# Kernel tuning notes

Measured on AMD Instinct MI355X. Metric: run time of the kernel, lower is better.

The kernel has to match this reference:

```python
import jax, jax.numpy as jnp
import numpy as np

STRIDE = 50
SIZES = (16.0, 32.0, 64.0)
RATIOS = (0.5, 1.0, 2.0)
THRESH = 0.95
IMG_H, IMG_W = 4200, 3200  # input is [N,1,IMG_H,IMG_W]


def _anchors(Hf, Wf):
    # torchvision-style anchors: 3 sizes x 3 aspect ratios = 9 per cell
    r = np.sqrt(np.array(RATIOS, dtype=np.float32))
    s = np.array(SIZES, dtype=np.float32)
    ws = (s[:, None] / r[None, :]).reshape(-1)  # [9]
    hs = (s[:, None] * r[None, :]).reshape(-1)  # [9]
    base = np.stack([-ws / 2, -hs / 2, ws / 2, hs / 2], axis=1)  # [9,4] x1,y1,x2,y2
    sx = (np.arange(Wf, dtype=np.float32) + 0.5) * STRIDE  # [Wf]
    sy = (np.arange(Hf, dtype=np.float32) + 0.5) * STRIDE  # [Hf]
    gx, gy = np.broadcast_arrays(sx[None, :], sy[:, None])  # [Hf,Wf]
    shift = np.stack([gx, gy, gx, gy], axis=-1)  # [Hf,Wf,4]
    return jnp.asarray(shift[:, :, None, :] + base[None, None, :, :])  # [Hf,Wf,9,4]


def _conv(x, w, b, stride, pad):
    y = jax.lax.conv_general_dilated(x, w, window_strides=stride, padding=pad,
                                     dimension_numbers=('NCHW', 'OIHW', 'NCHW'))
    return y + b[None, :, None, None]


def setup_inputs() -> dict:
    key = jax.random.key(0)
    ks = jax.random.split(key, 7)
    return {
        'X': jax.random.normal(ks[0], (8, 1, IMG_H, IMG_W), dtype=jnp.float32),
        'conv_w': jax.random.normal(ks[1], (2, 1, 50, 50), dtype=jnp.float32) * 0.02,
        'conv_b': jax.random.normal(ks[2], (2,), dtype=jnp.float32) * 0.02,
        'box_w': jax.random.normal(ks[3], (36, 2, 3, 3), dtype=jnp.float32) * 0.02,
        'box_b': jax.random.normal(ks[4], (36,), dtype=jnp.float32) * 0.02,
        'cls_w': jax.random.normal(ks[5], (2, 2, 3, 3), dtype=jnp.float32) * 0.5,
        'cls_b': jax.random.normal(ks[6], (2,), dtype=jnp.float32) * 0.5,
    }


def reference(X, conv_w, conv_b, box_w, box_b, cls_w, cls_b):
    feats = _conv(X, conv_w, conv_b, (STRIDE, STRIDE), 'VALID')        # [N,2,84,64]
    N, _, Hf, Wf = feats.shape
    off = _conv(feats, box_w, box_b, (1, 1), 'SAME')                   # [N,36,Hf,Wf]
    off = off.reshape(N, 9, 4, Hf, Wf).transpose(0, 3, 4, 1, 2)        # [N,Hf,Wf,9,4]
    cls = jax.nn.softmax(_conv(feats, cls_w, cls_b, (1, 1), 'SAME'), axis=1)  # Softmax2d
    mask = cls[:, 1] > THRESH                                          # [N,Hf,Wf]
    boxes = _anchors(Hf, Wf)[None] + off                               # offsets applied to anchors
    boxes = jnp.stack([
        jnp.clip(boxes[..., 0], 0.0, float(IMG_W)),
        jnp.clip(boxes[..., 1], 0.0, float(IMG_H)),
        jnp.clip(boxes[..., 2], 0.0, float(IMG_W)),
        jnp.clip(boxes[..., 3], 0.0, float(IMG_H)),
    ], axis=-1)
    # fixed-shape analogue of masked_select: zero out below-threshold anchors
    return boxes * mask[:, :, :, None, None].astype(boxes.dtype)
```

## Files before the change

kernel.cpp:

```cpp
#include <hip/hip_runtime.h>

#define IMG_H 4200
#define IMG_W 3200
#define HF 84
#define WF 64
#define NB 8

typedef const __attribute__((address_space(1))) unsigned int* gl_p;
typedef __attribute__((address_space(3))) unsigned int* lds_p;

__device__ __forceinline__ void gl_lds16(const void* g, void* l) {
    __builtin_amdgcn_global_load_lds((gl_p)g, (lds_p)l, 16, 0, 0);
}

__global__ __launch_bounds__(256) void conv1_kernel(
    const float* __restrict__ X, const float* __restrict__ cw,
    const float* __restrict__ cb, float* __restrict__ feats ) {
    __shared__ float2 w2[2500];
    __shared__ __align__(16) float4 rowbuf[2][800];
    __shared__ float2 part[3][WF];

    const int tid = threadIdx.x;
    const int wave = tid >> 6;
    const int lane = tid & 63;
    const int b = blockIdx.x;
    const int n = b / HF;
    const int i = b - n * HF;

    for (int e = tid; e < 2500; e += 256)
        w2[e] = make_float2(cw[e], cw[2500 + e]);

    const float* Xrow0 = X + ((size_t)n * IMG_H + (size_t)i * 50) * IMG_W;

    {
        const float4* s = (const float4*)Xrow0;
        gl_lds16(s + tid,       &rowbuf[0][tid]);
        gl_lds16(s + tid + 256, &rowbuf[0][tid + 256]);
        gl_lds16(s + tid + 512, &rowbuf[0][tid + 512]);
        if (tid < 32) gl_lds16(s + tid + 768, &rowbuf[0][tid + 768]);
    }
    __syncthreads();

    const int kx0 = wave * 12 + (wave < 2 ? wave : 2);
    const int len = (wave < 2) ? 13 : 12;
    float acc0 = 0.f, acc1 = 0.f;

    for (int ky = 0; ky < 50; ++ky) {
        const int cur = ky & 1;
        if (ky < 49) {
            const float4* s = (const float4*)(Xrow0 + (size_t)(ky + 1) * IMG_W);
            float4* d = rowbuf[cur ^ 1];
            gl_lds16(s + tid,       d + tid);
            gl_lds16(s + tid + 256, d + tid + 256);
            gl_lds16(s + tid + 512, d + tid + 512);
            if (tid < 32) gl_lds16(s + tid + 768, d + tid + 768);
        }
        const float* rowf = (const float*)rowbuf[cur];
        const float2* wrow = &w2[ky * 50];
#pragma unroll
        for (int t = 0; t < 13; ++t) {
            if (t < len) {
                const int kx = kx0 + t;
                const float xv = rowf[lane * 50 + kx];
                const float2 w = wrow[kx];
                acc0 = fmaf(xv, w.x, acc0);
                acc1 = fmaf(xv, w.y, acc1);
            }
        }
        __syncthreads();
    }

    if (wave > 0) part[wave - 1][lane] = make_float2(acc0, acc1);
    __syncthreads();
    if (wave == 0) {
#pragma unroll
        for (int w = 0; w < 3; ++w) {
            acc0 += part[w][lane].x;
            acc1 += part[w][lane].y;
        }
        ((float2*)feats)[(n * HF + i) * WF + lane] =
            make_float2(acc0 + cb[0], acc1 + cb[1]);
    }
}

__global__ __launch_bounds__(256) void head_kernel(
    const float* __restrict__ feats, const float* __restrict__ bw,
    const float* __restrict__ bb, const float* __restrict__ clw,
    const float* __restrict__ clb, float* __restrict__ out) {
    __shared__ float s_bw[648];
    __shared__ float s_bb[36];
    __shared__ float s_cw[36];
    __shared__ float s_cb[2];
    const int tid = threadIdx.x;
    for (int e = tid; e < 648; e += 256) s_bw[e] = bw[e];
    if (tid < 36) { s_bb[tid] = bb[tid]; s_cw[tid] = clw[tid]; }
    if (tid < 2) s_cb[tid] = clb[tid];
    __syncthreads();

    const int p = blockIdx.x * 256 + tid;
    const int j = p % WF;
    const int rem = p / WF;
    const int y = rem % HF;
    const int n = rem / HF;

    float f0[3][3], f1[3][3];
#pragma unroll
    for (int dy = 0; dy < 3; ++dy) {
        int yy = y + dy - 1;
#pragma unroll
        for (int dx = 0; dx < 3; ++dx) {
            int xx = j + dx - 1;
            float2 v = make_float2(0.f, 0.f);
            if (yy >= 0 && yy < HF && xx >= 0 && xx < WF)
                v = ((const float2*)feats)[(n * HF + yy) * WF + xx];
            f0[dy][dx] = v.x;
            f1[dy][dx] = v.y;
        }
    }

    float c0 = s_cb[0], c1 = s_cb[1];
#pragma unroll
    for (int ky = 0; ky < 3; ++ky)
#pragma unroll
        for (int kx = 0; kx < 3; ++kx) {
            int k = ky * 3 + kx;
            c0 = fmaf(f0[ky][kx], s_cw[k], c0);
            c0 = fmaf(f1[ky][kx], s_cw[9 + k], c0);
            c1 = fmaf(f0[ky][kx], s_cw[18 + k], c1);
            c1 = fmaf(f1[ky][kx], s_cw[27 + k], c1);
        }
    float mx = fmaxf(c0, c1);
    float e0 = expf(c0 - mx), e1 = expf(c1 - mx);
    float p1 = e1 / (e0 + e1);
    const float maskf = (p1 > 0.95f) ? 1.f : 0.f;

    const float gx = (j + 0.5f) * 50.f;
    const float gy = (y + 0.5f) * 50.f;
    const float wsv[9] = {22.627417f, 16.f, 11.3137085f,
                          45.254834f, 32.f, 22.627417f,
                          90.509668f, 64.f, 45.254834f};
    const float hsv[9] = {11.3137085f, 16.f, 22.627417f,
                          22.627417f, 32.f, 45.254834f,
                          45.254834f, 64.f, 90.509668f};

    float4* outp = (float4*)out + (size_t)p * 9;
#pragma unroll
    for (int a = 0; a < 9; ++a) {
        float o[4];
#pragma unroll
        for (int c = 0; c < 4; ++c) {
            const int ch = a * 4 + c;
            const float* w = &s_bw[ch * 18];
            float acc = s_bb[ch];
#pragma unroll
            for (int ky = 0; ky < 3; ++ky)
#pragma unroll
                for (int kx = 0; kx < 3; ++kx) {
                    int k = ky * 3 + kx;
                    acc = fmaf(f0[ky][kx], w[k], acc);
                    acc = fmaf(f1[ky][kx], w[9 + k], acc);
                }
            o[c] = acc;
        }
        const float hw = 0.5f * wsv[a], hh = 0.5f * hsv[a];
        float x1 = fminf(fmaxf(gx - hw + o[0], 0.f), 3200.f);
        float y1 = fminf(fmaxf(gy - hh + o[1], 0.f), 4200.f);
        float x2 = fminf(fmaxf(gx + hw + o[2], 0.f), 3200.f);
        float y2 = fminf(fmaxf(gy + hh + o[3], 0.f), 4200.f);
        outp[a] = make_float4(x1 * maskf, y1 * maskf, x2 * maskf, y2 * maskf);
    }
}

extern "C" void kernel_launch(void* const* d_in, const int* in_sizes, int n_in,
                              void* d_out, int out_size, void* d_ws, size_t ws_size,
                              hipStream_t stream) {
    const float* X   = (const float*)d_in[0];
    const float* cw  = (const float*)d_in[1];
    const float* cb  = (const float*)d_in[2];
    const float* bw  = (const float*)d_in[3];
    const float* bb  = (const float*)d_in[4];
    const float* clw = (const float*)d_in[5];
    const float* clb = (const float*)d_in[6];
    float* out = (float*)d_out;
    float* feats = (float*)d_ws;

    conv1_kernel<<<672, 256, 0, stream>>>(X, cw, cb, feats);
    head_kernel<<<168, 256, 0, stream>>>(feats, bw, bb, clw, clb, out);
}
```

Baseline: 576.9 us.

## Fuse conv1 and head into one banded kernel with halo feature recompute

Merges the strided 50x50 conv and the 3x3 head into one kernel, where each block computes a band of two feature rows plus halo rows in LDS and then emits boxes. This removes the global feature round trip and the second launch. Rows are streamed two at a time per stage to cut barrier count. The cost is recomputing halo feature rows, roughly doubling X reads and conv work, with fewer blocks in the grid.

```diff
diff --git a/kernel.cpp b/kernel.cpp
--- a/kernel.cpp
+++ b/kernel.cpp
@@ -5,6 +5,7 @@
 #define HF 84
 #define WF 64
 #define NB 8
+#define BAND 2
 
 typedef const __attribute__((address_space(1))) unsigned int* gl_p;
 typedef __attribute__((address_space(3))) unsigned int* lds_p;
@@ -13,161 +14,170 @@
     __builtin_amdgcn_global_load_lds((gl_p)g, (lds_p)l, 16, 0, 0);
 }
 
-__global__ __launch_bounds__(256) void conv1_kernel(
+__global__ __launch_bounds__(256) void fused_kernel(
     const float* __restrict__ X, const float* __restrict__ cw,
-    const float* __restrict__ cb, float* __restrict__ feats ) {
+    const float* __restrict__ cb, const float* __restrict__ bw,
+    const float* __restrict__ bb, const float* __restrict__ clw,
+    const float* __restrict__ clb, float* __restrict__ out) {
     __shared__ float2 w2[2500];
-    __shared__ __align__(16) float4 rowbuf[2][800];
+    __shared__ __align__(16) float4 rowbuf[2][1600];
+    __shared__ float2 feats[BAND + 2][WF];
     __shared__ float2 part[3][WF];
+    __shared__ float s_bw[648];
+    __shared__ float s_bb[36];
+    __shared__ float s_cw[36];
+    __shared__ float s_cb[2];
 
     const int tid = threadIdx.x;
     const int wave = tid >> 6;
     const int lane = tid & 63;
-    const int b = blockIdx.x;
-    const int n = b / HF;
-    const int i = b - n * HF;
+    const int n = blockIdx.y;
+    const int r0 = blockIdx.x * BAND;
 
-    for (int e = tid; e < 2500; e += 256)
-        w2[e] = make_float2(cw[e], cw[2500 + e]);
+    for (int e = tid; e < 2500; e += 256) w2[e] = make_float2(cw[e], cw[2500 + e]);
+    for (int e = tid; e < 648; e += 256) s_bw[e] = bw[e];
+    if (tid < 36) { s_bb[tid] = bb[tid]; s_cw[tid] = clw[tid]; }
+    if (tid < 2) s_cb[tid] = clb[tid];
+    ((float2*)feats)[tid] = make_float2(0.f, 0.f);
 
-    const float* Xrow0 = X + ((size_t)n * IMG_H + (size_t)i * 50) * IMG_W;
+    const int fr_lo = (r0 == 0) ? 0 : r0 - 1;
+    const int fr_hi = (r0 + BAND + 1 > HF) ? HF : r0 + BAND + 1;
+    const int ir0 = fr_lo * 50;
+    const int nst = (fr_hi * 50 - ir0) >> 1;
+
+    const float* Xb = X + ((size_t)n * IMG_H + ir0) * IMG_W;
 
     {
-        const float4* s = (const float4*)Xrow0;
-        gl_lds16(s + tid,       &rowbuf[0][tid]);
-        gl_lds16(s + tid + 256, &rowbuf[0][tid + 256]);
-        gl_lds16(s + tid + 512, &rowbuf[0][tid + 512]);
-        if (tid < 32) gl_lds16(s + tid + 768, &rowbuf[0][tid + 768]);
+        const float4* sp = (const float4*)Xb;
+        float4* d = rowbuf[0];
+#pragma unroll
+        for (int k = 0; k < 6; ++k) gl_lds16(sp + tid + 256 * k, d + tid + 256 * k);
+        if (tid < 64) gl_lds16(sp + tid + 1536, d + tid + 1536);
     }
     __syncthreads();
 
     const int kx0 = wave * 12 + (wave < 2 ? wave : 2);
     const int len = (wave < 2) ? 13 : 12;
-    float acc0 = 0.f, acc1 = 0.f;
+    const float cbias0 = cb[0], cbias1 = cb[1];
+    float a0 = 0.f, a1 = 0.f;
 
-    for (int ky = 0; ky < 50; ++ky) {
-        const int cur = ky & 1;
-        if (ky < 49) {
-            const float4* s = (const float4*)(Xrow0 + (size_t)(ky + 1) * IMG_W);
-            float4* d = rowbuf[cur ^ 1];
-            gl_lds16(s + tid,       d + tid);
-            gl_lds16(s + tid + 256, d + tid + 256);
-            gl_lds16(s + tid + 512, d + tid + 512);
-            if (tid < 32) gl_lds16(s + tid + 768, d + tid + 768);
+    for (int s = 0; s < nst; ++s) {
+        if (s + 1 < nst) {
+            const float4* sp = (const float4*)(Xb + (size_t)(s + 1) * 6400);
+            float4* d = rowbuf[(s + 1) & 1];
+#pragma unroll
+            for (int k = 0; k < 6; ++k) gl_lds16(sp + tid + 256 * k, d + tid + 256 * k);
+            if (tid < 64) gl_lds16(sp + tid + 1536, d + tid + 1536);
         }
-        const float* rowf = (const float*)rowbuf[cur];
-        const float2* wrow = &w2[ky * 50];
+        const float* rA = (const float*)rowbuf[s & 1];
+        const float* rB = rA + 3200;
+        const int ky2 = (ir0 + 2 * s) % 50;
+        const float2* wA = &w2[ky2 * 50];
+        const float2* wB = wA + 50;
 #pragma unroll
         for (int t = 0; t < 13; ++t) {
             if (t < len) {
                 const int kx = kx0 + t;
-                const float xv = rowf[lane * 50 + kx];
-                const float2 w = wrow[kx];
-                acc0 = fmaf(xv, w.x, acc0);
-                acc1 = fmaf(xv, w.y, acc1);
+                const float xa = rA[lane * 50 + kx];
+                const float2 wa = wA[kx];
+                a0 = fmaf(xa, wa.x, a0);
+                a1 = fmaf(xa, wa.y, a1);
             }
+        }
+#pragma unroll
+        for (int t = 0; t < 13; ++t) {
+            if (t < len) {
+                const int kx = kx0 + t;
+                const float xb = rB[lane * 50 + kx];
+                const float2 wb = wB[kx];
+                a0 = fmaf(xb, wb.x, a0);
+                a1 = fmaf(xb, wb.y, a1);
+            }
+        }
+        if (ky2 == 48) {
+            if (wave > 0) part[wave - 1][lane] = make_float2(a0, a1);
+            __syncthreads();
+            if (wave == 0) {
+                float s0 = a0, s1 = a1;
+#pragma unroll
+                for (int w = 0; w < 3; ++w) { s0 += part[w][lane].x; s1 += part[w][lane].y; }
+                const int fr = (ir0 + 2 * s) / 50;
+                feats[fr - r0 + 1][lane] = make_float2(s0 + cbias0, s1 + cbias1);
+            }
+            a0 = 0.f; a1 = 0.f;
         }
         __syncthreads();
     }
 
-    if (wave > 0) part[wave - 1][lane] = make_float2(acc0, acc1);
-    __syncthreads();
-    if (wave == 0) {
+    if (tid < BAND * WF) {
+        const int j = lane;
+        const int y = r0 + (tid >> 6);
+
+        float f0[3][3], f1[3][3];
 #pragma unroll
-        for (int w = 0; w < 3; ++w) {
-            acc0 += part[w][lane].x;
-            acc1 += part[w][lane].y;
+        for (int dy = 0; dy < 3; ++dy) {
+            const int q = (tid >> 6) + dy;
+#pragma unroll
+            for (int dx = 0; dx < 3; ++dx) {
+                const int xx = j + dx - 1;
+                float2 v = (xx >= 0 && xx < WF) ? feats[q][xx] : make_float2(0.f, 0.f);
+                f0[dy][dx] = v.x;
+                f1[dy][dx] = v.y;
+            }
         }
-        ((float2*)feats)[(n * HF + i) * WF + lane] =
-            make_float2(acc0 + cb[0], acc1 + cb[1]);
-    }
-}
 
-__global__ __launch_bounds__(256) void head_kernel(
-    const float* __restrict__ feats, const float* __restrict__ bw,
-    const float* __restrict__ bb, const float* __restrict__ clw,
-    const float* __restrict__ clb, float* __restrict__ out) {
-    __shared__ float s_bw[648];
-    __shared__ float s_bb[36];
-    __shared__ float s_cw[36];
-    __shared__ float s_cb[2];
-    const int tid = threadIdx.x;
-    for (int e = tid; e < 648; e += 256) s_bw[e] = bw[e];
-    if (tid < 36) { s_bb[tid] = bb[tid]; s_cw[tid] = clw[tid]; }
-    if (tid < 2) s_cb[tid] = clb[tid];
-    __syncthreads();
+        float c0 = s_cb[0], c1 = s_cb[1];
+#pragma unroll
+        for (int ky = 0; ky < 3; ++ky)
+#pragma unroll
+            for (int kx = 0; kx < 3; ++kx) {
+                int k = ky * 3 + kx;
+                c0 = fmaf(f0[ky][kx], s_cw[k], c0);
+                c0 = fmaf(f1[ky][kx], s_cw[9 + k], c0);
+                c1 = fmaf(f0[ky][kx], s_cw[18 + k], c1);
+                c1 = fmaf(f1[ky][kx], s_cw[27 + k], c1);
+            }
+        float mx = fmaxf(c0, c1);
+        float e0 = expf(c0 - mx), e1 = expf(c1 - mx);
+        float p1 = e1 / (e0 + e1);
+        const float maskf = (p1 > 0.95f) ? 1.f : 0.f;
 
-    const int p = blockIdx.x * 256 + tid;
-    const int j = p % WF;
-    const int rem = p / WF;
-    const int y = rem % HF;
-    const int n = rem / HF;
+        const float gx = (j + 0.5f) * 50.f;
+        const float gy = (y + 0.5f) * 50.f;
+        const float wsv[9] = {22.627417f, 16.f, 11.3137085f,
+                              45.254834f, 32.f, 22.627417f,
+                              90.509668f, 64.f, 45.254834f};
+        const float hsv[9] = {11.3137085f, 16.f, 22.627417f,
+                              22.627417f, 32.f, 45.254834f,
+                              45.254834f, 64.f, 90.509668f};
 
-    float f0[3][3], f1[3][3];
+        const int p = (n * HF + y) * WF + j;
+        float4* outp = (float4*)out + (size_t)p * 9;
 #pragma unroll
-    for (int dy = 0; dy < 3; ++dy) {
-        int yy = y + dy - 1;
+        for (int a = 0; a < 9; ++a) {
+            float o[4];
 #pragma unroll
-        for (int dx = 0; dx < 3; ++dx) {
-            int xx = j + dx - 1;
-            float2 v = make_float2(0.f, 0.f);
-            if (yy >= 0 && yy < HF && xx >= 0 && xx < WF)
-                v = ((const float2*)feats)[(n * HF + yy) * WF + xx];
-            f0[dy][dx] = v.x;
-            f1[dy][dx] = v.y;
+            for (int c = 0; c < 4; ++c) {
+                const int ch = a * 4 + c;
+                const float* w = &s_bw[ch * 18];
+                float acc = s_bb[ch];
+#pragma unroll
+                for (int ky = 0; ky < 3; ++ky)
+#pragma unroll
+                    for (int kx = 0; kx < 3; ++kx) {
+                        int k = ky * 3 + kx;
+                        acc = fmaf(f0[ky][kx], w[k], acc);
+                        acc = fmaf(f1[ky][kx], w[9 + k], acc);
+                    }
+                o[c] = acc;
+            }
+            const float hw = 0.5f * wsv[a], hh = 0.5f * hsv[a];
+            float x1 = fminf(fmaxf(gx - hw + o[0], 0.f), 3200.f);
+            float y1 = fminf(fmaxf(gy - hh + o[1], 0.f), 4200.f);
+            float x2 = fminf(fmaxf(gx + hw + o[2], 0.f), 3200.f);
+            float y2 = fminf(fmaxf(gy + hh + o[3], 0.f), 4200.f);
+            outp[a] = make_float4(x1 * maskf, y1 * maskf, x2 * maskf, y2 * maskf);
         }
-    }
-
-    float c0 = s_cb[0], c1 = s_cb[1];
-#pragma unroll
-    for (int ky = 0; ky < 3; ++ky)
-#pragma unroll
-        for (int kx = 0; kx < 3; ++kx) {
-            int k = ky * 3 + kx;
-            c0 = fmaf(f0[ky][kx], s_cw[k], c0);
-            c0 = fmaf(f1[ky][kx], s_cw[9 + k], c0);
-            c1 = fmaf(f0[ky][kx], s_cw[18 + k], c1);
-            c1 = fmaf(f1[ky][kx], s_cw[27 + k], c1);
-        }
-    float mx = fmaxf(c0, c1);
-    float e0 = expf(c0 - mx), e1 = expf(c1 - mx);
-    float p1 = e1 / (e0 + e1);
-    const float maskf = (p1 > 0.95f) ? 1.f : 0.f;
-
-    const float gx = (j + 0.5f) * 50.f;
-    const float gy = (y + 0.5f) * 50.f;
-    const float wsv[9] = {22.627417f, 16.f, 11.3137085f,
-                          45.254834f, 32.f, 22.627417f,
-                          90.509668f, 64.f, 45.254834f};
-    const float hsv[9] = {11.3137085f, 16.f, 22.627417f,
-                          22.627417f, 32.f, 45.254834f,
-                          45.254834f, 64.f, 90.509668f};
-
-    float4* outp = (float4*)out + (size_t)p * 9;
-#pragma unroll
-    for (int a = 0; a < 9; ++a) {
-        float o[4];
-#pragma unroll
-        for (int c = 0; c < 4; ++c) {
-            const int ch = a * 4 + c;
-            const float* w = &s_bw[ch * 18];
-            float acc = s_bb[ch];
-#pragma unroll
-            for (int ky = 0; ky < 3; ++ky)
-#pragma unroll
-                for (int kx = 0; kx < 3; ++kx) {
-                    int k = ky * 3 + kx;
-                    acc = fmaf(f0[ky][kx], w[k], acc);
-                    acc = fmaf(f1[ky][kx], w[9 + k], acc);
-                }
-            o[c] = acc;
-        }
-        const float hw = 0.5f * wsv[a], hh = 0.5f * hsv[a];
-        float x1 = fminf(fmaxf(gx - hw + o[0], 0.f), 3200.f);
-        float y1 = fminf(fmaxf(gy - hh + o[1], 0.f), 4200.f);
-        float x2 = fminf(fmaxf(gx + hw + o[2], 0.f), 3200.f);
-        float y2 = fminf(fmaxf(gy + hh + o[3], 0.f), 4200.f);
-        outp[a] = make_float4(x1 * maskf, y1 * maskf, x2 * maskf, y2 * maskf);
     }
 }
 
@@ -182,8 +192,7 @@
     const float* clw = (const float*)d_in[5];
     const float* clb = (const float*)d_in[6];
     float* out = (float*)d_out;
-    float* feats = (float*)d_ws;
+    (void)d_ws; (void)ws_size;
 
-    conv1_kernel<<<672, 256, 0, stream>>>(X, cw, cb, feats);
-    head_kernel<<<168, 256, 0, stream>>>(feats, bw, bb, clw, clb, out);
+    fused_kernel<<<dim3(HF / BAND, NB), 256, 0, stream>>>(X, cw, cb, bw, bb, clw, clb, out);
 }
```

Measured after the change: 651.2 us. 1.13x slower.
